# Kernel tuning notes

Hardware: AMD Instinct MI355X
Metric: run time of the kernel (lower is better)

The kernel has to match this reference:

```python
import jax, jax.numpy as jnp
import numpy as np

BH, BW = 4, 4  # bin_size_h, bin_size_w
BN_EPS = 1e-5


def _patch_split(t, bh, bw):
    # b c (bh ph) (bw pw) -> b (bh bw) (ph pw) c
    b, c, h, w = t.shape
    ph, pw = h // bh, w // bw
    t = t.reshape(b, c, bh, ph, bw, pw).transpose(0, 2, 4, 3, 5, 1)
    return t.reshape(b, bh * bw, ph * pw, c)


def _patch_recover(t, bh, bw, ph, pw):
    # b (bh bw) (ph pw) c -> b c (bh ph) (bw pw)
    b, n, p, c = t.shape
    t = t.reshape(b, bh, bw, ph, pw, c).transpose(0, 5, 1, 3, 2, 4)
    return t.reshape(b, c, bh * ph, bw * pw)


def setup_inputs() -> dict:
    key = jax.random.key(0)
    ks = jax.random.split(key, 16)
    b, C, h, w = 4, 512, 128, 128      # proj_dim = 512
    mid = C // 2                        # 256
    CM = 19 * 4                         # num_classes * num_local_prototype = 76
    return {
        "x": jax.random.normal(ks[0], (b, C, h, w), jnp.float32),
        "sim_mat": jax.random.normal(ks[1], (b, CM, h, w), jnp.float32),
        "global_cls_centers": jax.random.normal(ks[2], (19, 4, C), jnp.float32),
        "Wq": jax.random.normal(ks[3], (C, mid), jnp.float32) * 0.02,
        "bq": jax.random.normal(ks[4], (mid,), jnp.float32) * 0.02,
        "Wk": jax.random.normal(ks[5], (C, mid), jnp.float32) * 0.02,
        "bk": jax.random.normal(ks[6], (mid,), jnp.float32) * 0.02,
        "Wv": jax.random.normal(ks[7], (C, mid), jnp.float32) * 0.02,
        "bv": jax.random.normal(ks[8], (mid,), jnp.float32) * 0.02,
        "Wc": jax.random.normal(ks[9], (mid, C), jnp.float32) * 0.02,
        "bn_gamma": jax.random.uniform(ks[10], (C,), jnp.float32, 0.5, 1.5),
        "bn_beta": jax.random.normal(ks[11], (C,), jnp.float32) * 0.1,
        "bn_mean": jax.random.normal(ks[12], (C,), jnp.float32) * 0.1,
        "bn_var": jax.random.uniform(ks[13], (C,), jnp.float32, 0.5, 1.5),
    }


def reference(x, sim_mat, global_cls_centers, Wq, bq, Wk, bk, Wv, bv, Wc,
              bn_gamma, bn_beta, bn_mean, bn_var):
    b, C, h, w = x.shape
    CM = sim_mat.shape[1]
    ph, pw = h // BH, w // BW

    # pool_cam: adaptive avg pool to (BH, BW) == per-patch mean
    patch_cls_score = sim_mat.reshape(b, CM, BH, ph, BW, pw).mean(axis=(3, 5))  # [b,CM,BH,BW]

    sm = _patch_split(sim_mat, BH, BW)   # [b, N, P, CM]
    xs = _patch_split(x, BH, BW)         # [b, N, P, C]

    # patch_confidence: [b, N, CM, 1]
    conf = patch_cls_score.reshape(b, CM, BH * BW).transpose(0, 2, 1)[..., None]

    sm = jax.nn.softmax(sm, axis=2)      # softmax over pixels within patch
    local = jnp.einsum('bnpc,bnpk->bnck', sm, xs) * conf  # [b, N, CM, C]

    g = global_cls_centers.reshape(CM, C)  # (c m) k

    q = xs @ Wq + bq        # [b, N, P, mid]
    k = local @ Wk + bk     # [b, N, CM, mid]
    v = g @ Wv + bv         # [CM, mid] (identical across b, n -> broadcast)

    att = jax.nn.softmax(jnp.einsum('bnpm,bncm->bnpc', q, k), axis=-1)
    out = jnp.einsum('bnpc,cm->bnpm', att, v)               # [b, N, P, mid]

    out = _patch_recover(out, BH, BW, ph, pw)               # [b, mid, h, w]

    # conv_out: 1x1 conv (no bias) + BN (eval) + ReLU
    y = jnp.einsum('bmhw,mk->bkhw', out, Wc)
    inv = bn_gamma / jnp.sqrt(bn_var + BN_EPS)
    y = y * inv[None, :, None, None] + (bn_beta - bn_mean * inv)[None, :, None, None]
    y = jax.nn.relu(y)
    return (y, patch_cls_score)
```

## Files before the change

kernel.cpp:

```cpp
#include <hip/hip_runtime.h>

#define CM_    76
#define CMP_   80

typedef __attribute__((ext_vector_type(4))) float f32x4;
typedef __attribute__((ext_vector_type(8))) short bf16x8;

__device__ __forceinline__ unsigned short f2bf(float f) {
  union { float f; unsigned u; } v; v.f = f;
  unsigned r = v.u + 0x7FFFu + ((v.u >> 16) & 1u);
  return (unsigned short)(r >> 16);
}
__device__ __forceinline__ unsigned pack2(float a, float b) {
  return (unsigned)f2bf(a) | ((unsigned)f2bf(b) << 16);
}

#define OFF_BK2     0
#define OFF_INV     5120
#define OFF_ADD     5632
#define OFF_WKBQ    6144
#define OFF_BQKADD  6656
#define OFF_CBB     7168
#define OFF_EXPSIM  7172
#define OFF_LOCALBF 2628612
#define OFF_WQKT    3939332
#define OFF_VWT     5250052
#define OFF_WQWKT   5274628
#define OFF_WVWCT   5405700

__global__ __launch_bounds__(256) void kW_pre(
    const float* __restrict__ Wq, const float* __restrict__ Wk,
    const float* __restrict__ Wv, const float* __restrict__ Wc,
    const float* __restrict__ bq, const float* __restrict__ bk,
    const float* __restrict__ gamma, const float* __restrict__ beta,
    const float* __restrict__ mean, const float* __restrict__ var,
    unsigned short* __restrict__ WqWkT, unsigned short* __restrict__ WvWcT,
    float* __restrict__ wkbq, float* __restrict__ bqkadd,
    float* __restrict__ invp, float* __restrict__ addp, float* __restrict__ cbbp) {
  const int sel = blockIdx.y;
  if (blockIdx.x == 64) {
    const int c = sel * 256 + threadIdx.x;
    const float* wkr = Wk + (size_t)c * 256;
    const float* wqr = Wq + (size_t)c * 256;
    float s1 = 0.f, s2 = 0.f;
    for (int m = 0; m < 256; ++m) { s1 += wkr[m] * bq[m]; s2 += wqr[m] * bk[m]; }
    wkbq[c] = s1; bqkadd[c] = s2;
    float iv = gamma[c] * rsqrtf(var[c] + 1e-5f);
    invp[c] = iv; addp[c] = beta[c] - mean[c] * iv;
    if (c == 0) {
      float s = 0.f;
      for (int m = 0; m < 256; ++m) s += bq[m] * bk[m];
      cbbp[0] = s;
    }
    return;
  }
  const int r0 = (blockIdx.x >> 3) * 64, c0 = (blockIdx.x & 7) * 64;
  __shared__ __align__(16) unsigned short Asm[64 * 40];
  __shared__ __align__(16) unsigned short Bsm[64 * 40];
  const int t = threadIdx.x, lane = t & 63, w = t >> 6;
  const int lo = lane & 15, hi = lane >> 4;
  f32x4 acc[4];
#pragma unroll
  for (int cT = 0; cT < 4; ++cT) acc[cT] = (f32x4){0.f, 0.f, 0.f, 0.f};
  const float* Bsrc = sel ? Wv : Wk;
  for (int kc = 0; kc < 8; ++kc) {
    const int k0 = kc * 32;
    __syncthreads();
    {
      int nn = t >> 2, mq = (t & 3) * 8;
      const float* src = Bsrc + (size_t)(c0 + nn) * 256 + k0 + mq;
      float4 v0 = *(const float4*)src, v1 = *(const float4*)(src + 4);
      unsigned* d = (unsigned*)&Bsm[nn * 40 + mq];
      d[0] = pack2(v0.x, v0.y); d[1] = pack2(v0.z, v0.w);
      d[2] = pack2(v1.x, v1.y); d[3] = pack2(v1.z, v1.w);
    }
    if (sel == 0) {
      int r = t >> 2, mq = (t & 3) * 8;
      const float* src = Wq + (size_t)(r0 + r) * 256 + k0 + mq;
      float4 v0 = *(const float4*)src, v1 = *(const float4*)(src + 4);
      unsigned* d = (unsigned*)&Asm[r * 40 + mq];
      d[0] = pack2(v0.x, v0.y); d[1] = pack2(v0.z, v0.w);
      d[2] = pack2(v1.x, v1.y); d[3] = pack2(v1.z, v1.w);
    } else {
      int m = t >> 3, c2q = (t & 7) * 8;
      const float* src = Wc + (size_t)(k0 + m) * 512 + r0 + c2q;
      float4 v0 = *(const float4*)src, v1 = *(const float4*)(src + 4);
      Asm[(c2q + 0) * 40 + m] = f2bf(v0.x); Asm[(c2q + 1) * 40 + m] = f2bf(v0.y);
      Asm[(c2q + 2) * 40 + m] = f2bf(v0.z); Asm[(c2q + 3) * 40 + m] = f2bf(v0.w);
      Asm[(c2q + 4) * 40 + m] = f2bf(v1.x); Asm[(c2q + 5) * 40 + m] = f2bf(v1.y);
      Asm[(c2q + 6) * 40 + m] = f2bf(v1.z); Asm[(c2q + 7) * 40 + m] = f2bf(v1.w);
    }
    __syncthreads();
    bf16x8 afr = *(bf16x8*)(&Asm[(w * 16 + lo) * 40 + hi * 8]);
#pragma unroll
    for (int cT = 0; cT < 4; ++cT) {
      bf16x8 bfr = *(bf16x8*)(&Bsm[(cT * 16 + lo) * 40 + hi * 8]);
      acc[cT] = __builtin_amdgcn_mfma_f32_16x16x32_bf16(afr, bfr, acc[cT], 0, 0, 0);
    }
  }
  unsigned short* dst = sel ? WvWcT : WqWkT;
#pragma unroll
  for (int cT = 0; cT < 4; ++cT)
#pragma unroll
    for (int rr = 0; rr < 4; ++rr)
      dst[(size_t)(r0 + w * 16 + hi * 4 + rr) * 512 + c0 + cT * 16 + lo] = f2bf(acc[cT][rr]);
}

__global__ __launch_bounds__(256) void k1_stats(
    const float* __restrict__ sim, float* __restrict__ pcs,
    const float* __restrict__ cbbp,
    unsigned short* __restrict__ expsim, float* __restrict__ bk2) {
  const int cm = blockIdx.x, inst = blockIdx.y;
  const int t = threadIdx.x;
  unsigned short* erow = expsim + (size_t)inst * 81920 + (size_t)cm * 1024;
  if (cm >= CM_) {
    ((unsigned long long*)erow)[t] = 0ull;
    if (t == 0) bk2[inst * CMP_ + cm] = -1e30f;
    return;
  }
  const int b = inst >> 4, n = inst & 15, bh = n >> 2, bw = n & 3;
  const float* base = sim + ((size_t)(b * CM_ + cm) << 14);
  float v[4];
  float lsum = 0.f, lmax = -1e30f;
#pragma unroll
  for (int i = 0; i < 4; ++i) {
    int p = t + (i << 8);
    int pix = ((bh * 32 + (p >> 5)) << 7) + bw * 32 + (p & 31);
    float xv = base[pix];
    v[i] = xv; lsum += xv; lmax = fmaxf(lmax, xv);
  }
#pragma unroll
  for (int off = 32; off; off >>= 1) {
    lsum += __shfl_down(lsum, off);
    lmax = fmaxf(lmax, __shfl_down(lmax, off));
  }
  __shared__ float ssum[4], smax[4], bc[2];
  const int wid = t >> 6;
  if ((t & 63) == 0) { ssum[wid] = lsum; smax[wid] = lmax; }
  __syncthreads();
  if (t == 0) {
    bc[0] = ssum[0] + ssum[1] + ssum[2] + ssum[3];
    bc[1] = fmaxf(fmaxf(smax[0], smax[1]), fmaxf(smax[2], smax[3]));
  }
  __syncthreads();
  const float M = bc[1];
  float le = 0.f;
#pragma unroll
  for (int i = 0; i < 4; ++i) le += __expf(v[i] - M);
#pragma unroll
  for (int off = 32; off; off >>= 1) le += __shfl_down(le, off);
  if ((t & 63) == 0) ssum[wid] = le;
  __syncthreads();
  if (t == 0) {
    float E = ssum[0] + ssum[1] + ssum[2] + ssum[3];
    float conf = bc[0] * (1.f / 1024.f);
    pcs[((b * CM_ + cm) << 4) + n] = conf;
    bk2[inst * CMP_ + cm] = cbbp[0];
    bc[0] = conf / E;
  }
  __syncthreads();
  const float sc = bc[0];
#pragma unroll
  for (int i = 0; i < 4; ++i) {
    int p = t + (i << 8);
    erow[p] = f2bf(sc * __expf(v[i] - M));
  }
}

__global__ __launch_bounds__(256) void k2_local(
    const float* __restrict__ x, const unsigned short* __restrict__ expsim,
    const float* __restrict__ wkbq,
    unsigned short* __restrict__ local_bf, float* __restrict__ bk2) {
  const int cc = blockIdx.x, inst = blockIdx.y;
  const int b = inst >> 4, n = inst & 15, bh = n >> 2, bw = n & 3;
  const int t = threadIdx.x, lane = t & 63, w = t >> 6;
  const int lo = lane & 15, hi = lane >> 4;
  const int chw = cc * 64 + w * 16;
  const unsigned short* Abase = expsim + (size_t)inst * 81920;
  const float* xch = x + (((size_t)(b * 512 + chw + lo)) << 14) + bw * 32 + hi * 8;
  const int rowb = bh * 32;
  f32x4 acc[5];
#pragma unroll
  for (int T = 0; T < 5; ++T) acc[T] = (f32x4){0.f, 0.f, 0.f, 0.f};
#pragma unroll 4
  for (int ks = 0; ks < 32; ++ks) {
    const int k = ks * 32 + hi * 8;
    const float* xr = xch + ((size_t)(rowb + ks) << 7);
    float4 v0 = *(const float4*)(xr);
    float4 v1 = *(const float4*)(xr + 4);
    bf16x8 bfr;
    ((unsigned*)&bfr)[0] = pack2(v0.x, v0.y);
    ((unsigned*)&bfr)[1] = pack2(v0.z, v0.w);
    ((unsigned*)&bfr)[2] = pack2(v1.x, v1.y);
    ((unsigned*)&bfr)[3] = pack2(v1.z, v1.w);
#pragma unroll
    for (int T = 0; T < 5; ++T) {
      bf16x8 afr = *(const bf16x8*)(Abase + (size_t)(T * 16 + lo) * 1024 + k);
      acc[T] = __builtin_amdgcn_mfma_f32_16x16x32_bf16(afr, bfr, acc[T], 0, 0, 0);
    }
  }
  const float wk = wkbq[chw + lo];
#pragma unroll
  for (int T = 0; T < 5; ++T)
#pragma unroll
    for (int r = 0; r < 4; ++r) {
      int cm = T * 16 + hi * 4 + r;
      float av = acc[T][r];
      local_bf[((size_t)inst * CMP_ + cm) * 512 + chw + lo] = f2bf(av);
      float p = av * wk;
      p += __shfl_xor(p, 1); p += __shfl_xor(p, 2);
      p += __shfl_xor(p, 4); p += __shfl_xor(p, 8);
      if (lo == 0 && cm < CM_) atomicAdd(&bk2[inst * CMP_ + cm], p);
    }
}

__global__ __launch_bounds__(256) void k3n_wqkt(
    const unsigned short* __restrict__ local_bf, const unsigned short* __restrict__ WqWkT,
    const float* __restrict__ bqkadd, unsigned short* __restrict__ Wqkt) {
  const int blkc = blockIdx.x, inst = blockIdx.y;
  const int t = threadIdx.x, lane = t & 63, w = t >> 6;
  const int lo = lane & 15, hi = lane >> 4;
  const int cbase = blkc * 128 + w * 32;
  f32x4 acc[5][2];
#pragma unroll
  for (int cT = 0; cT < 2; ++cT) {
    float bv_ = bqkadd[cbase + cT * 16 + lo];
#pragma unroll
    for (int T = 0; T < 5; ++T) acc[T][cT] = (f32x4){bv_, bv_, bv_, bv_};
  }
  const unsigned short* Abase = local_bf + (size_t)inst * 40960;
#pragma unroll 4
  for (int ks = 0; ks < 16; ++ks) {
    const int k = ks * 32 + hi * 8;
    bf16x8 af[5];
#pragma unroll
    for (int T = 0; T < 5; ++T)
      af[T] = *(const bf16x8*)(Abase + (size_t)(T * 16 + lo) * 512 + k);
#pragma unroll
    for (int cT = 0; cT < 2; ++cT) {
      bf16x8 bfr = *(const bf16x8*)(WqWkT + (size_t)(cbase + cT * 16 + lo) * 512 + k);
#pragma unroll
      for (int T = 0; T < 5; ++T)
        acc[T][cT] = __builtin_amdgcn_mfma_f32_16x16x32_bf16(af[T], bfr, acc[T][cT], 0, 0, 0);
    }
  }
#pragma unroll
  for (int T = 0; T < 5; ++T)
#pragma unroll
    for (int cT = 0; cT < 2; ++cT)
#pragma unroll
      for (int r = 0; r < 4; ++r) {
        int cm = T * 16 + hi * 4 + r;
        Wqkt[(size_t)inst * 40960 + (size_t)cm * 512 + cbase + cT * 16 + lo] =
            f2bf(acc[T][cT][r]);
      }
}

__global__ __launch_bounds__(256) void kV_vwt(
    const unsigned short* __restrict__ WvWcT, const float* __restrict__ g,
    const float* __restrict__ bv, const float* __restrict__ Wc,
    unsigned short* __restrict__ vWt) {
  const int blk = blockIdx.x, half = blockIdx.y;
  const int t = threadIdx.x, lane = t & 63, w = t >> 6;
  const int lo = lane & 15, hi = lane >> 4;
  __shared__ float bvp[4][64];
  __shared__ float bvs[64];
  {
    int c2l = t & 63, part = t >> 6;
    float s = 0.f;
    for (int m = part * 64; m < part * 64 + 64; ++m)
      s += bv[m] * Wc[(size_t)m * 512 + blk * 64 + c2l];
    bvp[part][c2l] = s;
  }
  __syncthreads();
  if (t < 64) bvs[t] = bvp[0][t] + bvp[1][t] + bvp[2][t] + bvp[3][t];
  __syncthreads();
  const int r2 = blk * 64 + w * 16;
  f32x4 acc[3];
#pragma unroll
  for (int j = 0; j < 3; ++j) acc[j] = (f32x4){0.f, 0.f, 0.f, 0.f};
#pragma unroll 4
  for (int ks = 0; ks < 16; ++ks) {
    const int k = ks * 32 + hi * 8;
    bf16x8 afr = *(const bf16x8*)(WvWcT + (size_t)(r2 + lo) * 512 + k);
#pragma unroll
    for (int j = 0; j < 3; ++j) {
      int cm = (half * 3 + j) * 16 + lo;
      cm = cm > 75 ? 75 : cm;
      const float* gr = g + (size_t)cm * 512 + k;
      float4 v0 = *(const float4*)gr, v1 = *(const float4*)(gr + 4);
      bf16x8 bfr;
      ((unsigned*)&bfr)[0] = pack2(v0.x, v0.y);
      ((unsigned*)&bfr)[1] = pack2(v0.z, v0.w);
      ((unsigned*)&bfr)[2] = pack2(v1.x, v1.y);
      ((unsigned*)&bfr)[3] = pack2(v1.z, v1.w);
      acc[j] = __builtin_amdgcn_mfma_f32_16x16x32_bf16(afr, bfr, acc[j], 0, 0, 0);
    }
  }
#pragma unroll
  for (int j = 0; j < 3; ++j)
#pragma unroll
    for (int rr = 0; rr < 4; ++rr) {
      int c2g = blk * 64 + w * 16 + hi * 4 + rr;
      vWt[(size_t)c2g * 96 + (half * 3 + j) * 16 + lo] =
          f2bf(acc[j][rr] + bvs[w * 16 + hi * 4 + rr]);
    }
}

__global__ __launch_bounds__(256) void k4_attn(
    const float* __restrict__ x, const unsigned short* __restrict__ Wqkt,
    const float* __restrict__ bk2, const unsigned short* __restrict__ vWt,
    const float* __restrict__ inv_arr, const float* __restrict__ add_arr,
    float* __restrict__ y) {
  const int pt = blockIdx.x, inst = blockIdx.y;
  const int b = inst >> 4, n = inst & 15, bh = n >> 2, bw = n & 3;
  __shared__ unsigned short Xs[4][32 * 72];
  __shared__ unsigned short Att[4][32 * 96];
  __shared__ float bn_s[1024];
  const int t = threadIdx.x, lane = t & 63, w = t >> 6;
  const int lo = lane & 15, hi = lane >> 4;
  const int pq = lane & 7, chp0 = lane >> 3;

  for (int i = t; i < 512; i += 256) { bn_s[i] = inv_arr[i]; bn_s[512 + i] = add_arr[i]; }

  const int imgrow = bh * 32 + pt * 4 + w;
  const size_t pixbase = (size_t)imgrow * 128 + bw * 32;
  const size_t xrowbase = (((size_t)b * 512) << 14) + pixbase;
  const unsigned short* Wi = Wqkt + (size_t)inst * 40960;

  f32x4 acc[2][5];
#pragma unroll
  for (int T = 0; T < 5; ++T) {
    f32x4 bv;
#pragma unroll
    for (int r = 0; r < 4; ++r) bv[r] = bk2[inst * CMP_ + T * 16 + hi * 4 + r];
    acc[0][T] = bv; acc[1][T] = bv;
  }

  for (int kc = 0; kc < 8; ++kc) {
#pragma unroll
    for (int i = 0; i < 4; ++i) {
      int chp = chp0 + i * 8;
      int ch = kc * 64 + chp * 2;
      const float* xa = x + xrowbase + ((size_t)ch << 14) + pq * 4;
      float4 va = *(const float4*)(xa);
      float4 vb = *(const float4*)(xa + 16384);
      unsigned short* dst = &Xs[w][(pq * 4) * 72 + chp * 2];
      *(unsigned*)(dst + 0 * 72) = pack2(va.x, vb.x);
      *(unsigned*)(dst + 1 * 72) = pack2(va.y, vb.y);
      *(unsigned*)(dst + 2 * 72) = pack2(va.z, vb.z);
      *(unsigned*)(dst + 3 * 72) = pack2(va.w, vb.w);
    }
#pragma unroll
    for (int ks = 0; ks < 2; ++ks) {
      int kb = kc * 64 + ks * 32 + hi * 8;
      bf16x8 b0 = *(bf16x8*)(&Xs[w][lo * 72 + ks * 32 + hi * 8]);
      bf16x8 b1 = *(bf16x8*)(&Xs[w][(16 + lo) * 72 + ks * 32 + hi * 8]);
#pragma unroll
      for (int T = 0; T < 5; ++T) {
        bf16x8 afr = *(const bf16x8*)(Wi + (size_t)(T * 16 + lo) * 512 + kb);
        acc[0][T] = __builtin_amdgcn_mfma_f32_16x16x32_bf16(afr, b0, acc[0][T], 0, 0, 0);
        acc[1][T] = __builtin_amdgcn_mfma_f32_16x16x32_bf16(afr, b1, acc[1][T], 0, 0, 0);
      }
    }
  }

#pragma unroll
  for (int p = 0; p < 2; ++p) {
    float m = -1e30f;
#pragma unroll
    for (int T = 0; T < 5; ++T)
#pragma unroll
      for (int r = 0; r < 4; ++r) m = fmaxf(m, acc[p][T][r]);
    m = fmaxf(m, __shfl_xor(m, 16));
    m = fmaxf(m, __shfl_xor(m, 32));
    float e[5][4];
    float s = 0.f;
#pragma unroll
    for (int T = 0; T < 5; ++T)
#pragma unroll
      for (int r = 0; r < 4; ++r) { float ev = __expf(acc[p][T][r] - m); e[T][r] = ev; s += ev; }
    s += __shfl_xor(s, 16);
    s += __shfl_xor(s, 32);
    float rinv = 1.f / s;
    int px = p * 16 + lo;
#pragma unroll
    for (int T = 0; T < 5; ++T) {
      unsigned l32 = pack2(e[T][0] * rinv, e[T][1] * rinv);
      unsigned h32 = pack2(e[T][2] * rinv, e[T][3] * rinv);
      *(unsigned long long*)(&Att[w][px * 96 + T * 16 + hi * 4]) =
          (unsigned long long)l32 | ((unsigned long long)h32 << 32);
    }
    *(unsigned long long*)(&Att[w][px * 96 + 80 + hi * 4]) = 0ull;
  }

  __syncthreads();

  bf16x8 bfr3[2][3];
#pragma unroll
  for (int p = 0; p < 2; ++p)
#pragma unroll
    for (int ks = 0; ks < 3; ++ks)
      bfr3[p][ks] = *(bf16x8*)(&Att[w][(p * 16 + lo) * 96 + ks * 32 + hi * 8]);

  for (int cT = 0; cT < 32; ++cT) {
    f32x4 a0 = (f32x4){0.f, 0.f, 0.f, 0.f}, a1 = a0;
    const unsigned short* vr = vWt + (size_t)(cT * 16 + lo) * 96;
#pragma unroll
    for (int ks = 0; ks < 3; ++ks) {
      bf16x8 afr = *(const bf16x8*)(vr + ks * 32 + hi * 8);
      a0 = __builtin_amdgcn_mfma_f32_16x16x32_bf16(afr, bfr3[0][ks], a0, 0, 0, 0);
      a1 = __builtin_amdgcn_mfma_f32_16x16x32_bf16(afr, bfr3[1][ks], a1, 0, 0, 0);
    }
    f32x4 inv4 = *(f32x4*)(&bn_s[cT * 16 + hi * 4]);
    f32x4 add4 = *(f32x4*)(&bn_s[512 + cT * 16 + hi * 4]);
#pragma unroll
    for (int r = 0; r < 4; ++r) {
      int ch = cT * 16 + hi * 4 + r;
      float v0 = fmaxf(a0[r] * inv4[r] + add4[r], 0.f);
      float v1 = fmaxf(a1[r] * inv4[r] + add4[r], 0.f);
      size_t yb = (((size_t)(b * 512 + ch)) << 14) + pixbase;
      y[yb + lo] = v0;
      y[yb + 16 + lo] = v1;
    }
  }
}

extern "C" void kernel_launch(void* const* d_in, const int* in_sizes, int n_in,
                              void* d_out, int out_size, void* d_ws, size_t ws_size,
                              hipStream_t stream) {
  (void)in_sizes; (void)n_in; (void)out_size; (void)ws_size;
  const float* x     = (const float*)d_in[0];
  const float* sim   = (const float*)d_in[1];
  const float* g     = (const float*)d_in[2];
  const float* Wq    = (const float*)d_in[3];
  const float* bq    = (const float*)d_in[4];
  const float* Wk    = (const float*)d_in[5];
  const float* bk    = (const float*)d_in[6];
  const float* Wv    = (const float*)d_in[7];
  const float* bv    = (const float*)d_in[8];
  const float* Wc    = (const float*)d_in[9];
  const float* gamma = (const float*)d_in[10];
  const float* beta  = (const float*)d_in[11];
  const float* mean  = (const float*)d_in[12];
  const float* var   = (const float*)d_in[13];
  float* out = (float*)d_out;
  float* ws  = (float*)d_ws;
  float* y   = out;
  float* pcs = out + 33554432;
  unsigned short* expsim  = (unsigned short*)(ws + OFF_EXPSIM);
  unsigned short* localbf = (unsigned short*)(ws + OFF_LOCALBF);
  unsigned short* Wqkt    = (unsigned short*)(ws + OFF_WQKT);
  unsigned short* vWt     = (unsigned short*)(ws + OFF_VWT);
  unsigned short* WqWkT   = (unsigned short*)(ws + OFF_WQWKT);
  unsigned short* WvWcT   = (unsigned short*)(ws + OFF_WVWCT);

  hipLaunchKernelGGL(kW_pre, dim3(65, 2), dim3(256), 0, stream,
                     Wq, Wk, Wv, Wc, bq, bk, gamma, beta, mean, var,
                     WqWkT, WvWcT, ws + OFF_WKBQ, ws + OFF_BQKADD,
                     ws + OFF_INV, ws + OFF_ADD, ws + OFF_CBB);
  hipLaunchKernelGGL(k1_stats, dim3(CMP_, 64), dim3(256), 0, stream,
                     sim, pcs, ws + OFF_CBB, expsim, ws + OFF_BK2);
  hipLaunchKernelGGL(k2_local, dim3(8, 64), dim3(256), 0, stream,
                     x, expsim, ws + OFF_WKBQ, localbf, ws + OFF_BK2);
  hipLaunchKernelGGL(k3n_wqkt, dim3(4, 64), dim3(256), 0, stream,
                     localbf, WqWkT, ws + OFF_BQKADD, Wqkt);
  hipLaunchKernelGGL(kV_vwt, dim3(8, 2), dim3(256), 0, stream,
                     WvWcT, g, bv, Wc, vWt);
  hipLaunchKernelGGL(k4_attn, dim3(8, 64), dim3(256), 0, stream,
                     x, Wqkt, ws + OFF_BK2, vWt,
                     ws + OFF_INV, ws + OFF_ADD, y);
}
```

Measured before the change: 423.1 us.

## Split-K k2_local across four wave groups and halve k3n tile width

k2_local now runs 1024 threads per block. Four K-slices each accumulate a partial MFMA result, then the partials are summed through shared memory before the epilogue. k3n_wqkt drops from two column tiles per wave to one and doubles the grid. Both changes are meant to raise wave-level parallelism on two small launch grids (512 and 256 blocks), at the cost of an LDS reduction plus a block-wide barrier in k2. They also remove the reuse of A fragments across column tiles in k3n.

```diff
diff --git a/kernel.cpp b/kernel.cpp
--- a/kernel.cpp
+++ b/kernel.cpp
@@ -167,23 +167,25 @@
   }
 }
 
-__global__ __launch_bounds__(256) void k2_local(
+__global__ __launch_bounds__(1024, 8) void k2_local(
     const float* __restrict__ x, const unsigned short* __restrict__ expsim,
     const float* __restrict__ wkbq,
     unsigned short* __restrict__ local_bf, float* __restrict__ bk2) {
   const int cc = blockIdx.x, inst = blockIdx.y;
   const int b = inst >> 4, n = inst & 15, bh = n >> 2, bw = n & 3;
   const int t = threadIdx.x, lane = t & 63, w = t >> 6;
+  const int g = w & 3, kh = w >> 2;
   const int lo = lane & 15, hi = lane >> 4;
-  const int chw = cc * 64 + w * 16;
+  const int chw = cc * 64 + g * 16;
   const unsigned short* Abase = expsim + (size_t)inst * 81920;
   const float* xch = x + (((size_t)(b * 512 + chw + lo)) << 14) + bw * 32 + hi * 8;
   const int rowb = bh * 32;
+  __shared__ float red[3][4][5][4][64];
   f32x4 acc[5];
 #pragma unroll
   for (int T = 0; T < 5; ++T) acc[T] = (f32x4){0.f, 0.f, 0.f, 0.f};
 #pragma unroll 4
-  for (int ks = 0; ks < 32; ++ks) {
+  for (int ks = kh * 8; ks < kh * 8 + 8; ++ks) {
     const int k = ks * 32 + hi * 8;
     const float* xr = xch + ((size_t)(rowb + ks) << 7);
     float4 v0 = *(const float4*)(xr);
@@ -199,19 +201,33 @@
       acc[T] = __builtin_amdgcn_mfma_f32_16x16x32_bf16(afr, bfr, acc[T], 0, 0, 0);
     }
   }
-  const float wk = wkbq[chw + lo];
-#pragma unroll
-  for (int T = 0; T < 5; ++T)
-#pragma unroll
-    for (int r = 0; r < 4; ++r) {
-      int cm = T * 16 + hi * 4 + r;
-      float av = acc[T][r];
-      local_bf[((size_t)inst * CMP_ + cm) * 512 + chw + lo] = f2bf(av);
-      float p = av * wk;
-      p += __shfl_xor(p, 1); p += __shfl_xor(p, 2);
-      p += __shfl_xor(p, 4); p += __shfl_xor(p, 8);
-      if (lo == 0 && cm < CM_) atomicAdd(&bk2[inst * CMP_ + cm], p);
-    }
+  if (kh) {
+#pragma unroll
+    for (int T = 0; T < 5; ++T)
+#pragma unroll
+      for (int r = 0; r < 4; ++r) red[kh - 1][g][T][r][lane] = acc[T][r];
+  }
+  __syncthreads();
+  if (kh == 0) {
+#pragma unroll
+    for (int T = 0; T < 5; ++T)
+#pragma unroll
+      for (int r = 0; r < 4; ++r)
+        acc[T][r] += red[0][g][T][r][lane] + red[1][g][T][r][lane] + red[2][g][T][r][lane];
+    const float wk = wkbq[chw + lo];
+#pragma unroll
+    for (int T = 0; T < 5; ++T)
+#pragma unroll
+      for (int r = 0; r < 4; ++r) {
+        int cm = T * 16 + hi * 4 + r;
+        float av = acc[T][r];
+        local_bf[((size_t)inst * CMP_ + cm) * 512 + chw + lo] = f2bf(av);
+        float p = av * wk;
+        p += __shfl_xor(p, 1); p += __shfl_xor(p, 2);
+        p += __shfl_xor(p, 4); p += __shfl_xor(p, 8);
+        if (lo == 0 && cm < CM_) atomicAdd(&bk2[inst * CMP_ + cm], p);
+      }
+  }
 }
 
 __global__ __launch_bounds__(256) void k3n_wqkt(
@@ -220,40 +236,31 @@
   const int blkc = blockIdx.x, inst = blockIdx.y;
   const int t = threadIdx.x, lane = t & 63, w = t >> 6;
   const int lo = lane & 15, hi = lane >> 4;
-  const int cbase = blkc * 128 + w * 32;
-  f32x4 acc[5][2];
-#pragma unroll
-  for (int cT = 0; cT < 2; ++cT) {
-    float bv_ = bqkadd[cbase + cT * 16 + lo];
-#pragma unroll
-    for (int T = 0; T < 5; ++T) acc[T][cT] = (f32x4){bv_, bv_, bv_, bv_};
+  const int cbase = blkc * 64 + w * 16;
+  f32x4 acc[5];
+  {
+    float bv_ = bqkadd[cbase + lo];
+#pragma unroll
+    for (int T = 0; T < 5; ++T) acc[T] = (f32x4){bv_, bv_, bv_, bv_};
   }
   const unsigned short* Abase = local_bf + (size_t)inst * 40960;
 #pragma unroll 4
   for (int ks = 0; ks < 16; ++ks) {
     const int k = ks * 32 + hi * 8;
-    bf16x8 af[5];
-#pragma unroll
-    for (int T = 0; T < 5; ++T)
-      af[T] = *(const bf16x8*)(Abase + (size_t)(T * 16 + lo) * 512 + k);
-#pragma unroll
-    for (int cT = 0; cT < 2; ++cT) {
-      bf16x8 bfr = *(const bf16x8*)(WqWkT + (size_t)(cbase + cT * 16 + lo) * 512 + k);
-#pragma unroll
-      for (int T = 0; T < 5; ++T)
-        acc[T][cT] = __builtin_amdgcn_mfma_f32_16x16x32_bf16(af[T], bfr, acc[T][cT], 0, 0, 0);
+    bf16x8 bfr = *(const bf16x8*)(WqWkT + (size_t)(cbase + lo) * 512 + k);
+#pragma unroll
+    for (int T = 0; T < 5; ++T) {
+      bf16x8 af = *(const bf16x8*)(Abase + (size_t)(T * 16 + lo) * 512 + k);
+      acc[T] = __builtin_amdgcn_mfma_f32_16x16x32_bf16(af, bfr, acc[T], 0, 0, 0);
     }
   }
 #pragma unroll
   for (int T = 0; T < 5; ++T)
 #pragma unroll
-    for (int cT = 0; cT < 2; ++cT)
-#pragma unroll
-      for (int r = 0; r < 4; ++r) {
-        int cm = T * 16 + hi * 4 + r;
-        Wqkt[(size_t)inst * 40960 + (size_t)cm * 512 + cbase + cT * 16 + lo] =
-            f2bf(acc[T][cT][r]);
-      }
+    for (int r = 0; r < 4; ++r) {
+      int cm = T * 16 + hi * 4 + r;
+      Wqkt[(size_t)inst * 40960 + (size_t)cm * 512 + cbase + lo] = f2bf(acc[T][r]);
+    }
 }
 
 __global__ __launch_bounds__(256) void kV_vwt(
@@ -461,9 +468,9 @@
                      ws + OFF_INV, ws + OFF_ADD, ws + OFF_CBB);
   hipLaunchKernelGGL(k1_stats, dim3(CMP_, 64), dim3(256), 0, stream,
                      sim, pcs, ws + OFF_CBB, expsim, ws + OFF_BK2);
-  hipLaunchKernelGGL(k2_local, dim3(8, 64), dim3(256), 0, stream,
+  hipLaunchKernelGGL(k2_local, dim3(8, 64), dim3(1024), 0, stream,
                      x, expsim, ws + OFF_WKBQ, localbf, ws + OFF_BK2);
-  hipLaunchKernelGGL(k3n_wqkt, dim3(4, 64), dim3(256), 0, stream,
+  hipLaunchKernelGGL(k3n_wqkt, dim3(8, 64), dim3(256), 0, stream,
                      localbf, WqWkT, ws + OFF_BQKADD, Wqkt);
   hipLaunchKernelGGL(kV_vwt, dim3(8, 2), dim3(256), 0, stream,
                      WvWcT, g, bv, Wc, vWt);
```

After: 461.4 us. 9.1% more time.

## Stage k2_local operands through double-buffered LDS via direct global-to-LDS loads

Applied to the files above, without the earlier changes.

Rewrites the k2_local GEMM loop so each block of 512 threads covers 128 channels and stages the x tile and expsim tile into swizzled, double-buffered shared memory using global_load_lds, prefetching the next k-step while MFMAs consume the current one. The expsim A-tile is now loaded once per block and shared across 8 waves instead of each wave reading it from global memory, and the grid is halved. The cost is an extra barrier per iteration, more LDS use that may reduce occupancy, and XOR swizzle indexing that has to be correct.

```diff
diff --git a/kernel.cpp b/kernel.cpp
--- a/kernel.cpp
+++ b/kernel.cpp
@@ -14,6 +14,11 @@
 __device__ __forceinline__ unsigned pack2(float a, float b) {
   return (unsigned)f2bf(a) | ((unsigned)f2bf(b) << 16);
 }
+
+#define GLOAD_LDS16(gsrc, ldst)                                                      \
+  __builtin_amdgcn_global_load_lds(                                                  \
+      (const __attribute__((address_space(1))) void*)(gsrc),                         \
+      (__attribute__((address_space(3))) void*)(ldst), 16, 0, 0)
 
 #define OFF_BK2     0
 #define OFF_INV     5120
@@ -167,7 +172,7 @@
   }
 }
 
-__global__ __launch_bounds__(256) void k2_local(
+__global__ __launch_bounds__(512) void k2_local(
     const float* __restrict__ x, const unsigned short* __restrict__ expsim,
     const float* __restrict__ wkbq,
     unsigned short* __restrict__ local_bf, float* __restrict__ bk2) {
@@ -175,30 +180,63 @@
   const int b = inst >> 4, n = inst & 15, bh = n >> 2, bw = n & 3;
   const int t = threadIdx.x, lane = t & 63, w = t >> 6;
   const int lo = lane & 15, hi = lane >> 4;
-  const int chw = cc * 64 + w * 16;
-  const unsigned short* Abase = expsim + (size_t)inst * 81920;
-  const float* xch = x + (((size_t)(b * 512 + chw + lo)) << 14) + bw * 32 + hi * 8;
-  const int rowb = bh * 32;
+  const int chw = cc * 128 + w * 16;
+
+  __shared__ __align__(16) unsigned char AsB[2][80 * 64];
+  __shared__ __align__(16) unsigned char BsB[2][128 * 128];
+
+  const int bq_ = ((lane & 7) ^ (lane >> 3)) * 4;
+  const float* pB0 = x + (((size_t)(b * 512 + cc * 128 + w * 16 + 0 + (lane >> 3))) << 14)
+                       + (size_t)(bh * 32) * 128 + bw * 32 + bq_;
+  const float* pB1 = x + (((size_t)(b * 512 + cc * 128 + w * 16 + 8 + (lane >> 3))) << 14)
+                       + (size_t)(bh * 32) * 128 + bw * 32 + bq_;
+  const unsigned short* pA = expsim + (size_t)inst * 81920
+                           + (size_t)(w * 16 + (lane >> 2)) * 1024
+                           + ((lane & 3) ^ ((lane >> 2) & 3)) * 8;
+
+  const int brow = (w * 16 + lo) * 128;
+  const int bs0 = (((hi << 1) | 0) ^ (lo & 7)) << 4;
+  const int bs1 = (((hi << 1) | 1) ^ (lo & 7)) << 4;
+  const int aoff = (hi ^ (lo & 3)) << 4;
+
   f32x4 acc[5];
 #pragma unroll
   for (int T = 0; T < 5; ++T) acc[T] = (f32x4){0.f, 0.f, 0.f, 0.f};
-#pragma unroll 4
-  for (int ks = 0; ks < 32; ++ks) {
-    const int k = ks * 32 + hi * 8;
-    const float* xr = xch + ((size_t)(rowb + ks) << 7);
-    float4 v0 = *(const float4*)(xr);
-    float4 v1 = *(const float4*)(xr + 4);
-    bf16x8 bfr;
-    ((unsigned*)&bfr)[0] = pack2(v0.x, v0.y);
-    ((unsigned*)&bfr)[1] = pack2(v0.z, v0.w);
-    ((unsigned*)&bfr)[2] = pack2(v1.x, v1.y);
-    ((unsigned*)&bfr)[3] = pack2(v1.z, v1.w);
-#pragma unroll
-    for (int T = 0; T < 5; ++T) {
-      bf16x8 afr = *(const bf16x8*)(Abase + (size_t)(T * 16 + lo) * 1024 + k);
-      acc[T] = __builtin_amdgcn_mfma_f32_16x16x32_bf16(afr, bfr, acc[T], 0, 0, 0);
-    }
-  }
+
+  GLOAD_LDS16(pB0, &BsB[0][(w * 16 + 0) * 128]);
+  GLOAD_LDS16(pB1, &BsB[0][(w * 16 + 8) * 128]);
+  if (w < 5) GLOAD_LDS16(pA, &AsB[0][w * 1024]);
+  pB0 += 128; pB1 += 128; pA += 32;
+  __syncthreads();
+
+  for (int tt = 0; tt < 32; ++tt) {
+    const int cur = tt & 1;
+    if (tt < 31) {
+      const int nxt = cur ^ 1;
+      GLOAD_LDS16(pB0, &BsB[nxt][(w * 16 + 0) * 128]);
+      GLOAD_LDS16(pB1, &BsB[nxt][(w * 16 + 8) * 128]);
+      if (w < 5) GLOAD_LDS16(pA, &AsB[nxt][w * 1024]);
+      pB0 += 128; pB1 += 128; pA += 32;
+    }
+    {
+      const unsigned char* BsP = BsB[cur];
+      const unsigned char* AsP = AsB[cur];
+      float4 v0 = *(const float4*)(BsP + brow + bs0);
+      float4 v1 = *(const float4*)(BsP + brow + bs1);
+      bf16x8 bfr;
+      ((unsigned*)&bfr)[0] = pack2(v0.x, v0.y);
+      ((unsigned*)&bfr)[1] = pack2(v0.z, v0.w);
+      ((unsigned*)&bfr)[2] = pack2(v1.x, v1.y);
+      ((unsigned*)&bfr)[3] = pack2(v1.z, v1.w);
+#pragma unroll
+      for (int T = 0; T < 5; ++T) {
+        bf16x8 afr = *(const bf16x8*)(AsP + ((T * 16 + lo) << 6) + aoff);
+        acc[T] = __builtin_amdgcn_mfma_f32_16x16x32_bf16(afr, bfr, acc[T], 0, 0, 0);
+      }
+    }
+    __syncthreads();
+  }
+
   const float wk = wkbq[chw + lo];
 #pragma unroll
   for (int T = 0; T < 5; ++T)
@@ -461,7 +499,7 @@
                      ws + OFF_INV, ws + OFF_ADD, ws + OFF_CBB);
   hipLaunchKernelGGL(k1_stats, dim3(CMP_, 64), dim3(256), 0, stream,
                      sim, pcs, ws + OFF_CBB, expsim, ws + OFF_BK2);
-  hipLaunchKernelGGL(k2_local, dim3(8, 64), dim3(256), 0, stream,
+  hipLaunchKernelGGL(k2_local, dim3(4, 64), dim3(512), 0, stream,
                      x, expsim, ws + OFF_WKBQ, localbf, ws + OFF_BK2);
   hipLaunchKernelGGL(k3n_wqkt, dim3(4, 64), dim3(256), 0, stream,
                      localbf, WqWkT, ws + OFF_BQKADD, Wqkt);
```

Result: faster. 404.7 us (-4.3%).

## Stage k2_local operands through double-buffered LDS via global_load_lds with full-row x loads

Applied to the files above, without the earlier changes.

Restructures k2_local so each 512-thread block covers a full patch row (4 patches) and 32 channels. The expsim and x tiles are copied into double-buffered, XOR-swizzled shared memory using direct global-to-LDS loads, and the MFMA fragments are then read from LDS. The goal is coalesced full 128-float row reads of x instead of scattered 32-byte chunks, plus overlap of the next tile's loads with the current compute. In exchange it uses more LDS per block, adds a barrier every iteration, and changes the grid to 16x16 blocks, which may lower occupancy.

```diff
diff --git a/kernel.cpp b/kernel.cpp
--- a/kernel.cpp
+++ b/kernel.cpp
@@ -14,6 +14,11 @@
 __device__ __forceinline__ unsigned pack2(float a, float b) {
   return (unsigned)f2bf(a) | ((unsigned)f2bf(b) << 16);
 }
+
+#define GLOAD_LDS16(gsrc, ldst)                                                      \
+  __builtin_amdgcn_global_load_lds(                                                  \
+      (const __attribute__((address_space(1))) void*)(gsrc),                         \
+      (__attribute__((address_space(3))) void*)(ldst), 16, 0, 0)
 
 #define OFF_BK2     0
 #define OFF_INV     5120
@@ -167,38 +172,79 @@
   }
 }
 
-__global__ __launch_bounds__(256) void k2_local(
+__global__ __launch_bounds__(512) void k2_local(
     const float* __restrict__ x, const unsigned short* __restrict__ expsim,
     const float* __restrict__ wkbq,
     unsigned short* __restrict__ local_bf, float* __restrict__ bk2) {
-  const int cc = blockIdx.x, inst = blockIdx.y;
-  const int b = inst >> 4, n = inst & 15, bh = n >> 2, bw = n & 3;
+  const int chb = blockIdx.x;
+  const int sb  = blockIdx.y;
+  const int b = sb >> 2, bh = sb & 3;
   const int t = threadIdx.x, lane = t & 63, w = t >> 6;
   const int lo = lane & 15, hi = lane >> 4;
-  const int chw = cc * 64 + w * 16;
-  const unsigned short* Abase = expsim + (size_t)inst * 81920;
-  const float* xch = x + (((size_t)(b * 512 + chw + lo)) << 14) + bw * 32 + hi * 8;
-  const int rowb = bh * 32;
+  const int bw = w >> 1, ct = w & 1;
+  const int inst = b * 16 + bh * 4 + bw;
+  const int chw = chb * 32 + ct * 16;
+
+  __shared__ __align__(16) unsigned char As_[2][4][80 * 64];
+  __shared__ __align__(16) unsigned char Bs_[2][32 * 512];
+
+  const int chA = 4 * w + 0 + (lane >> 5);
+  const int chB = 4 * w + 2 + (lane >> 5);
+  const float* pB0 = x + (((size_t)(b * 512 + chb * 32 + chA)) << 14)
+                       + (size_t)(bh * 32) * 128 + (size_t)(((lane & 31) ^ (chA & 31)) * 4);
+  const float* pB1 = x + (((size_t)(b * 512 + chb * 32 + chB)) << 14)
+                       + (size_t)(bh * 32) * 128 + (size_t)(((lane & 31) ^ (chB & 31)) * 4);
+  const int ka = ct ? 3 : 0, kb_ = ct ? 4 : 1;
+  const unsigned short* eb = expsim + (size_t)inst * 81920
+                           + (size_t)(lane >> 2) * 1024
+                           + (size_t)(((lane & 3) ^ ((lane >> 2) & 3)) * 8);
+  const unsigned short* pA0 = eb + (size_t)(ka * 16) * 1024;
+  const unsigned short* pA1 = eb + (size_t)(kb_ * 16) * 1024;
+  const unsigned short* pA2 = eb + (size_t)(2 * 16) * 1024;
+
+  const int chl = ct * 16 + lo;
+  const int ps0 = (((8 * bw + 2 * hi) | 0) ^ (chl & 31)) * 16;
+  const int ps1 = (((8 * bw + 2 * hi) | 1) ^ (chl & 31)) * 16;
+  const int aoff = (hi ^ (lo & 3)) * 16;
+
   f32x4 acc[5];
 #pragma unroll
   for (int T = 0; T < 5; ++T) acc[T] = (f32x4){0.f, 0.f, 0.f, 0.f};
-#pragma unroll 4
-  for (int ks = 0; ks < 32; ++ks) {
-    const int k = ks * 32 + hi * 8;
-    const float* xr = xch + ((size_t)(rowb + ks) << 7);
-    float4 v0 = *(const float4*)(xr);
-    float4 v1 = *(const float4*)(xr + 4);
-    bf16x8 bfr;
-    ((unsigned*)&bfr)[0] = pack2(v0.x, v0.y);
-    ((unsigned*)&bfr)[1] = pack2(v0.z, v0.w);
-    ((unsigned*)&bfr)[2] = pack2(v1.x, v1.y);
-    ((unsigned*)&bfr)[3] = pack2(v1.z, v1.w);
-#pragma unroll
-    for (int T = 0; T < 5; ++T) {
-      bf16x8 afr = *(const bf16x8*)(Abase + (size_t)(T * 16 + lo) * 1024 + k);
-      acc[T] = __builtin_amdgcn_mfma_f32_16x16x32_bf16(afr, bfr, acc[T], 0, 0, 0);
-    }
-  }
+
+  auto STAGE = [&](int bufi) {
+    GLOAD_LDS16(pB0, &Bs_[bufi][(4 * w + 0) * 512]);
+    GLOAD_LDS16(pB1, &Bs_[bufi][(4 * w + 2) * 512]);
+    GLOAD_LDS16(pA0, &As_[bufi][bw][ka * 1024]);
+    GLOAD_LDS16(pA1, &As_[bufi][bw][kb_ * 1024]);
+    if (ct == 0) GLOAD_LDS16(pA2, &As_[bufi][bw][2 * 1024]);
+    pB0 += 128; pB1 += 128; pA0 += 32; pA1 += 32; pA2 += 32;
+  };
+
+  STAGE(0);
+  __syncthreads();
+
+  for (int tt = 0; tt < 32; ++tt) {
+    const int cur = tt & 1;
+    if (tt < 31) STAGE(cur ^ 1);
+    {
+      const unsigned char* Bp = Bs_[cur] + chl * 512;
+      float4 v0 = *(const float4*)(Bp + ps0);
+      float4 v1 = *(const float4*)(Bp + ps1);
+      bf16x8 bfr;
+      ((unsigned*)&bfr)[0] = pack2(v0.x, v0.y);
+      ((unsigned*)&bfr)[1] = pack2(v0.z, v0.w);
+      ((unsigned*)&bfr)[2] = pack2(v1.x, v1.y);
+      ((unsigned*)&bfr)[3] = pack2(v1.z, v1.w);
+      const unsigned char* Ap = As_[cur][bw];
+#pragma unroll
+      for (int T = 0; T < 5; ++T) {
+        bf16x8 afr = *(const bf16x8*)(Ap + ((T * 16 + lo) << 6) + aoff);
+        acc[T] = __builtin_amdgcn_mfma_f32_16x16x32_bf16(afr, bfr, acc[T], 0, 0, 0);
+      }
+    }
+    __syncthreads();
+  }
+
   const float wk = wkbq[chw + lo];
 #pragma unroll
   for (int T = 0; T < 5; ++T)
@@ -461,7 +507,7 @@
                      ws + OFF_INV, ws + OFF_ADD, ws + OFF_CBB);
   hipLaunchKernelGGL(k1_stats, dim3(CMP_, 64), dim3(256), 0, stream,
                      sim, pcs, ws + OFF_CBB, expsim, ws + OFF_BK2);
-  hipLaunchKernelGGL(k2_local, dim3(8, 64), dim3(256), 0, stream,
+  hipLaunchKernelGGL(k2_local, dim3(16, 16), dim3(512), 0, stream,
                      x, expsim, ws + OFF_WKBQ, localbf, ws + OFF_BK2);
   hipLaunchKernelGGL(k3n_wqkt, dim3(4, 64), dim3(256), 0, stream,
                      localbf, WqWkT, ws + OFF_BQKADD, Wqkt);
```

Measured after the change: 420.9 us. About the same (-0.5%).
